# Kernel optimization log

Hardware: AMD Instinct MI355X
Metric: run time of the kernel (lower is better)

The kernel has to match this reference:

```python
import jax, jax.numpy as jnp
import numpy as np
from functools import partial

GRAD_THR = 0.01
COUNT_THR = 3
MIN_PROB = 0.1
MAX_PROB = 0.9
FREE_PROB = 1e-10
HEIGHT_Q = 0.7


def prob2logodds(p):
    return jnp.log(p) - jnp.log1p(-p)


def shift_diff(x, d):
    # right neighbor minus left neighbor at dilation d (replicate padding on width)
    xp = jnp.pad(x, [(0, 0)] * (x.ndim - 1) + [(d, d)], mode='edge')
    return xp[..., 2 * d:] - xp[..., :-2 * d]


def assign_score(depth):
    rml_dx = jax.nn.relu(shift_diff(depth, 1))    # relu(right - left)
    lmr_dx = jax.nn.relu(-shift_diff(depth, 1))   # relu(left - right)
    rml_ddx = jax.nn.relu(-shift_diff(rml_dx, 2))  # relu(-(right-left))
    lmr_ddx = jax.nn.relu(shift_diff(lmr_dx, 2))   # relu(-(left-right))
    W = depth.shape[-1]
    grad_pos = jnp.concatenate([rml_ddx[..., :W // 2], lmr_ddx[..., W // 2:]], axis=-1)
    grad_neg = jnp.concatenate([lmr_ddx[..., :W // 2], rml_ddx[..., W // 2:]], axis=-1)
    return grad_pos, grad_neg


def _occupancy_one(xyz, score, g_mask, size, grad_thr, count_thr):
    # xyz: [3, N]; score, g_mask: [N]
    x, y, z = xyz[0], xyz[1], xyz[2]
    range_mask = (x >= 0) & (x <= size - 1) & (z >= 0) & (z <= size - 1)
    height_mask = y < jnp.quantile(y, HEIGHT_Q)
    valid = height_mask & range_mask
    obj = valid & (~g_mask) & (score > 0)
    ground = valid & g_mask
    xi = jnp.clip(x.astype(jnp.int32), 0, size - 1)
    zi = jnp.clip(z.astype(jnp.int32), 0, size - 1)
    idx = xi + size * zi  # [N] flat grid index
    G = size * size
    occ = jnp.zeros(G, jnp.float32).at[idx].add(
        jnp.where(obj & (score > grad_thr), 1.0, 0.0))
    norm = jnp.zeros(G, jnp.float32).at[idx].add(obj.astype(jnp.float32))
    gcnt = jnp.zeros(G, jnp.float32).at[idx].add(ground.astype(jnp.float32))
    free = (gcnt > 0) & (norm == 0)
    unknown = (~free) & (norm < count_thr)
    prob = occ / jnp.maximum(norm, 1.0)
    prob = jnp.where(unknown | free, 0.5, prob)
    return prob, free, unknown


def compute_occupancy_probability(scaled_ptcloud, ground_flat, disc_flat, size, grad_thr, count_thr):
    f = partial(_occupancy_one, size=size, grad_thr=grad_thr, count_thr=count_thr)
    return jax.vmap(f)(scaled_ptcloud, disc_flat, ground_flat)


def max_pool3x3(x):
    return jax.lax.reduce_window(
        x, -jnp.inf, jax.lax.max,
        (1, 1, 3, 3), (1, 1, 1, 1),
        [(0, 0), (0, 0), (1, 1), (1, 1)])


def setup_inputs() -> dict:
    key = jax.random.key(0)
    k1, k2, k3 = jax.random.split(key, 3)
    B, H, W, S = 32, 384, 1280, 256
    N = H * W
    depth = jax.random.uniform(k1, (B, 1, H, W), jnp.float32, 0.1, 80.0)
    ptc = jax.random.uniform(k2, (B, 3, N), jnp.float32, -5.0, float(S) + 5.0)
    gmask = jax.random.randint(k3, (B, 1, H, W), 0, 2).astype(bool)
    return {"depth": depth, "scaled_ptcloud": ptc, "ground_mask": gmask, "ogm_size": S}


def reference(depth, scaled_ptcloud, ground_mask, ogm_size):
    B = depth.shape[0]
    S = ogm_size
    prior_free_odds = prob2logodds(FREE_PROB)
    p_min_odds = prob2logodds(MIN_PROB)
    p_max_odds = prob2logodds(MAX_PROB)
    n_max_odds = prob2logodds(MAX_PROB)

    grad_pos, grad_neg = assign_score(depth)
    gp_flat = grad_pos.reshape(B, -1)
    gn_flat = grad_neg.reshape(B, -1)
    gm_flat = ground_mask.reshape(B, -1)

    pos_prob, free, unknown = compute_occupancy_probability(
        scaled_ptcloud, gm_flat, gp_flat, S, GRAD_THR, COUNT_THR)
    pos_odds = prob2logodds(pos_prob)
    pos_odds = jnp.where(free, prior_free_odds, pos_odds)
    pos_odds = jnp.where(unknown, 0.0, pos_odds)
    pos_odds = jnp.clip(pos_odds, p_min_odds, p_max_odds)

    neg_prob, _, _ = compute_occupancy_probability(
        scaled_ptcloud, gm_flat, gn_flat, S, GRAD_THR, COUNT_THR)
    neg_odds = prob2logodds(neg_prob)
    neg_odds = jnp.where(free | unknown, 0.0, neg_odds)
    neg_odds = jnp.clip(neg_odds, 0.0, n_max_odds)
    neg_odds = max_pool3x3(neg_odds.reshape(B, 1, S, S))

    return pos_odds.reshape(B, 1, S, S) - neg_odds
```

## Files before the change

kernel.cpp:

```cpp
#include <hip/hip_runtime.h>
#include <stdint.h>

#define H_    384
#define W_    1280
#define NPTS  (H_ * W_)
#define S_    256
#define G_    (S_ * S_)
#define NBX   32
#define NBINS 4096
#define QCAP  4096
#define NT_Q  1024
#define LO_   (-16.0f)
#define INVW_ (4096.0f / 544.0f)
#define PMAX  2.1972246f

typedef unsigned int u32;
typedef unsigned long long u64;
typedef unsigned char u8;

__device__ __forceinline__ u32 fkey(float f) {
    u32 u = __float_as_uint(f);
    return (u & 0x80000000u) ? ~u : (u | 0x80000000u);
}
__device__ __forceinline__ float keyfloat(u32 k) {
    u32 u = (k & 0x80000000u) ? (k ^ 0x80000000u) : ~k;
    return __uint_as_float(u);
}
__device__ __forceinline__ int lbin(float y) {
    int b = (int)floorf((y - LO_) * INVW_);
    return b < 0 ? 0 : (b > NBINS - 1 ? NBINS - 1 : b);
}

__global__ void k_histlin(const float* __restrict__ ptc, const u8* __restrict__ gmb,
                          u32* __restrict__ hg, u32* __restrict__ mode) {
    __shared__ u32 h[NBINS];
    const int t = threadIdx.x, b = blockIdx.y;
    if (blockIdx.x == 0 && b == 0 && t < 64) {
        u32 v = ((const u32*)gmb)[t];
        bool bad = !(v == 0u || v == 1u || v == 0x3F800000u);
        u64 m = __ballot(bad);
        if (t == 0) *mode = (m == 0ULL) ? 1u : 0u;
    }
    for (int j = t; j < NBINS; j += 256) h[j] = 0u;
    __syncthreads();
    const float4* y4 = (const float4*)(ptc + (size_t)b * 3 * NPTS + NPTS);
    for (int i = blockIdx.x * 256 + t; i < NPTS / 4; i += NBX * 256) {
        float4 v = y4[i];
        atomicAdd(&h[lbin(v.x)], 1u);
        atomicAdd(&h[lbin(v.y)], 1u);
        atomicAdd(&h[lbin(v.z)], 1u);
        atomicAdd(&h[lbin(v.w)], 1u);
    }
    __syncthreads();
    u32* dst = hg + ((size_t)b * NBX + blockIdx.x) * NBINS;
    for (int j = t; j < NBINS; j += 256) dst[j] = h[j];
}

__global__ __launch_bounds__(NT_Q) void k_quant(const float* __restrict__ ptc,
                                                const u32* __restrict__ hg,
                                                float* __restrict__ tbuf,
                                                int ka, float wlo, float whi) {
    __shared__ u32 h[NBINS];
    __shared__ u32 part[NT_Q];
    __shared__ u32 bufA[QCAP];
    __shared__ u32 bufB[QCAP];
    __shared__ u32 sres[6];
    __shared__ u32 ca, cb;
    const int t = threadIdx.x, b = blockIdx.x;

    for (int j = t; j < NBINS; j += NT_Q) {
        u32 s = 0;
        for (int k = 0; k < NBX; k++) s += hg[((size_t)b * NBX + k) * NBINS + j];
        h[j] = s;
    }
    if (t == 0) { ca = 0u; cb = 0u; }
    __syncthreads();

    u32 loc = 0;
#pragma unroll
    for (int q = 0; q < NBINS / NT_Q; q++) loc += h[t * (NBINS / NT_Q) + q];
    part[t] = loc;
    __syncthreads();
    for (int ofs = 1; ofs < NT_Q; ofs <<= 1) {
        u32 v = (t >= ofs) ? part[t - ofs] : 0u;
        __syncthreads();
        part[t] += v;
        __syncthreads();
    }
    u32 before = part[t] - loc;
    const u32 ra = (u32)ka, rb = (u32)ka + 1u;
#pragma unroll
    for (int q = 0; q < NBINS / NT_Q; q++) {
        const int j = t * (NBINS / NT_Q) + q;
        const u32 v = h[j];
        if (before <= ra && ra < before + v) { sres[0] = (u32)j; sres[1] = ra - before; }
        if (before <= rb && rb < before + v) { sres[2] = (u32)j; sres[3] = rb - before; }
        before += v;
    }
    __syncthreads();
    const int binA = (int)sres[0], binB = (int)sres[2];
    const u32 remA = sres[1], remB = sres[3];
    const bool twob = (binB != binA);

    const float4* y4 = (const float4*)(ptc + (size_t)b * 3 * NPTS + NPTS);
    for (int i = t; i < NPTS / 4; i += NT_Q) {
        float4 v = y4[i];
        float f[4] = {v.x, v.y, v.z, v.w};
#pragma unroll
        for (int q = 0; q < 4; q++) {
            const int bn = lbin(f[q]);
            if (bn == binA) {
                u32 p = atomicAdd(&ca, 1u);
                if (p < QCAP) bufA[p] = fkey(f[q]);
            } else if (twob && bn == binB) {
                u32 p = atomicAdd(&cb, 1u);
                if (p < QCAP) bufB[p] = fkey(f[q]);
            }
        }
    }
    __syncthreads();

    const u32 mA = ca < QCAP ? ca : QCAP;
    for (u32 i = t; i < mA; i += NT_Q) {
        const u32 k = bufA[i];
        u32 less = 0, eq = 0;
        for (u32 j = 0; j < mA; j++) { u32 kj = bufA[j]; less += (kj < k); eq += (kj == k); }
        if (less <= remA && remA < less + eq) sres[4] = k;
    }
    const u32* src = twob ? bufB : bufA;
    const u32 mB = twob ? (cb < QCAP ? cb : QCAP) : mA;
    for (u32 i = t; i < mB; i += NT_Q) {
        const u32 k = src[i];
        u32 less = 0, eq = 0;
        for (u32 j = 0; j < mB; j++) { u32 kj = src[j]; less += (kj < k); eq += (kj == k); }
        if (less <= remB && remB < less + eq) sres[5] = k;
    }
    __syncthreads();
    if (t == 0) {
        float ylo = keyfloat(sres[4]);
        float yhi = keyfloat(sres[5]);
        tbuf[b] = __fadd_rn(__fmul_rn(ylo, wlo), __fmul_rn(yhi, whi));
    }
}

__global__ void k_scatter(const float* __restrict__ depth, const float* __restrict__ ptc,
                          const u8* __restrict__ gmb, const float* __restrict__ tbuf,
                          const u32* __restrict__ mode,
                          u64* __restrict__ pk, u8* __restrict__ gflag) {
    __shared__ float st;
    __shared__ u32 smode;
    if (threadIdx.x == 0) { st = tbuf[blockIdx.y]; smode = *mode; }
    __syncthreads();
    const int b = blockIdx.y;
    const int i = blockIdx.x * 256 + threadIdx.x;
    const size_t pb = (size_t)b * 3 * NPTS;
    const float y = ptc[pb + NPTS + i];
    if (!(y < st)) return;
    const float x = ptc[pb + i];
    const float z = ptc[pb + 2 * NPTS + i];
    if (!(x >= 0.0f && x <= 255.0f && z >= 0.0f && z <= 255.0f)) return;
    const int cell = (int)x + S_ * (int)z;

    u32 g;
    if (smode) g = ((const u32*)gmb)[(size_t)b * NPTS + i];
    else       g = (u32)gmb[(size_t)b * NPTS + i];

    if (g) { gflag[(size_t)b * G_ + cell] = 1; return; }

    const int col = i % W_;
    const int r0  = i - col;
    int j1 = col - 2; if (j1 < 0) j1 = 0;
    int j2 = col + 2; if (j2 > W_ - 1) j2 = W_ - 1;
    int am = j1 - 1;  if (am < 0) am = 0;
    int ap = j1 + 1;  if (ap > W_ - 1) ap = W_ - 1;
    int bm = j2 - 1;  if (bm < 0) bm = 0;
    int bp = j2 + 1;  if (bp > W_ - 1) bp = W_ - 1;
    const float* drow = depth + (size_t)b * NPTS + r0;
    float a = drow[ap] - drow[am];
    float c = drow[bp] - drow[bm];
    float rml1 = fmaxf(a, 0.0f),  lmr1 = fmaxf(-a, 0.0f);
    float rml2 = fmaxf(c, 0.0f),  lmr2 = fmaxf(-c, 0.0f);
    float rddx = fmaxf(rml1 - rml2, 0.0f);
    float lddx = fmaxf(lmr2 - lmr1, 0.0f);
    float sp, sn;
    if (col < W_ / 2) { sp = rddx; sn = lddx; } else { sp = lddx; sn = rddx; }
    u64 p = (sp > 0.0f) ? (1ULL | ((u64)(sp > 0.01f) << 12)) : 0ULL;
    u64 n = (sn > 0.0f) ? ((1ULL << 24) | ((u64)(sn > 0.01f) << 36)) : 0ULL;
    const u64 inc = p | n;
    if (inc) atomicAdd(&pk[(size_t)b * G_ + cell], inc);
}

#define TX 64
#define TZ 16

__device__ __forceinline__ float neg_val(u64 w) {
    const u32 pn = (u32)w & 0xFFFu;
    if (pn < 3u) return 0.0f;
    const u32 nn = (u32)(w >> 24) & 0xFFFu;
    if (nn < 3u) return 0.0f;
    const u32 no = (u32)(w >> 36) & 0xFFFu;
    float p = (float)no / (float)nn;
    float v = logf(p) - log1pf(-p);
    return fminf(fmaxf(v, 0.0f), PMAX);
}

__global__ void k_finalpool(const u64* __restrict__ pk, const u8* __restrict__ gflag,
                            float* __restrict__ out) {
    __shared__ float ng[(TZ + 2) * (TX + 2)];
    const int t = threadIdx.x, b = blockIdx.y;
    const int x0 = (blockIdx.x & 3) * TX;
    const int z0 = (blockIdx.x >> 2) * TZ;
    const u64* pkb = pk + (size_t)b * G_;
    const u8* gfb = gflag + (size_t)b * G_;
    for (int idx = t; idx < (TZ + 2) * (TX + 2); idx += 256) {
        const int gx = x0 + idx % (TX + 2) - 1;
        const int gz = z0 + idx / (TX + 2) - 1;
        float v = -INFINITY;
        if (gx >= 0 && gx < S_ && gz >= 0 && gz < S_) v = neg_val(pkb[gx + S_ * gz]);
        ng[idx] = v;
    }
    __syncthreads();
    const int lx = t & 63;
    const int lz0 = (t >> 6) * 4;
#pragma unroll
    for (int k = 0; k < 4; k++) {
        const int lz = lz0 + k;
        const int cell = (x0 + lx) + S_ * (z0 + lz);
        const u64 w = pkb[cell];
        const u32 pn = (u32)w & 0xFFFu;
        float po;
        if (pn < 3u) {
            po = (pn == 0u && gfb[cell]) ? -PMAX : 0.0f;
        } else {
            const u32 oc = (u32)(w >> 12) & 0xFFFu;
            float p = (float)oc / (float)pn;
            float v = logf(p) - log1pf(-p);
            po = fminf(fmaxf(v, -PMAX), PMAX);
        }
        float mx = -INFINITY;
#pragma unroll
        for (int dz = 0; dz < 3; dz++)
#pragma unroll
            for (int dx = 0; dx < 3; dx++)
                mx = fmaxf(mx, ng[(lz + dz) * (TX + 2) + (lx + dx)]);
        out[(size_t)b * G_ + cell] = po - mx;
    }
}

extern "C" void kernel_launch(void* const* d_in, const int* in_sizes, int n_in,
                              void* d_out, int out_size, void* d_ws, size_t ws_size,
                              hipStream_t stream) {
    const float* depth = (const float*)d_in[0];
    const float* ptc   = (const float*)d_in[1];
    const u8* gm       = (const u8*)d_in[2];
    const int B = in_sizes[0] / NPTS;

    char* ws = (char*)d_ws;
    size_t off = 0;
    auto alloc = [&](size_t bytes) -> void* {
        void* p = ws + off; off += (bytes + 255) & ~(size_t)255; return p;
    };
    u64* pk     = (u64*)alloc((size_t)B * G_ * 8);
    u8*  gflag  = (u8*)alloc((size_t)B * G_);
    const size_t zero_bytes = off;
    u32* hg     = (u32*)alloc((size_t)B * NBX * NBINS * 4);
    float* tbuf = (float*)alloc((size_t)B * 4);
    u32* mode   = (u32*)alloc(4);
    (void)ws_size;

    hipMemsetAsync(d_ws, 0, zero_bytes, stream);

    const float idxf = 0.7f * (float)(NPTS - 1);
    const int   ka   = (int)floorf(idxf);
    const float whi  = idxf - (float)ka;
    const float wlo  = 1.0f - whi;

    k_histlin <<<dim3(NBX, B), dim3(256), 0, stream>>>(ptc, gm, hg, mode);
    k_quant   <<<dim3(B), dim3(NT_Q), 0, stream>>>(ptc, hg, tbuf, ka, wlo, whi);
    k_scatter <<<dim3(NPTS / 256, B), dim3(256), 0, stream>>>(
        depth, ptc, gm, tbuf, mode, pk, gflag);
    k_finalpool<<<dim3(64, B), dim3(256), 0, stream>>>(pk, gflag, (float*)d_out);
}
```

Measured before the change: 535.2 us.

## Split quantile selection into parallel collect/select kernels and pack counters in u32

The single-block-per-batch quantile kernel is split into four stages. A global atomic histogram merge replaces the per-block partial histograms, a small prefix-search kernel finds the bins, a multi-block pass collects candidate keys into global buffers, and a select kernel ranks them from shared memory. This removes the serial full-point-cloud scan done by one block per batch. The scatter kernel now processes four points per thread with vector nontemporal loads. Cell counters are packed into 32-bit words with 8-bit fields instead of 64-bit words with 12-bit fields, which risks overflow if a cell receives 256 or more points. QCAP is also halved.

```diff
diff --git a/kernel.cpp b/kernel.cpp
--- a/kernel.cpp
+++ b/kernel.cpp
@@ -8,8 +8,7 @@
 #define G_    (S_ * S_)
 #define NBX   32
 #define NBINS 4096
-#define QCAP  4096
-#define NT_Q  1024
+#define QCAP  2048
 #define LO_   (-16.0f)
 #define INVW_ (4096.0f / 544.0f)
 #define PMAX  2.1972246f
@@ -17,6 +16,8 @@
 typedef unsigned int u32;
 typedef unsigned long long u64;
 typedef unsigned char u8;
+typedef float f32x4 __attribute__((ext_vector_type(4)));
+typedef u32   u32x4 __attribute__((ext_vector_type(4)));
 
 __device__ __forceinline__ u32 fkey(float f) {
     u32 u = __float_as_uint(f);
@@ -32,7 +33,7 @@
 }
 
 __global__ void k_histlin(const float* __restrict__ ptc, const u8* __restrict__ gmb,
-                          u32* __restrict__ hg, u32* __restrict__ mode) {
+                          u32* __restrict__ hgsum, u32* __restrict__ mode) {
     __shared__ u32 h[NBINS];
     const int t = threadIdx.x, b = blockIdx.y;
     if (blockIdx.x == 0 && b == 0 && t < 64) {
@@ -43,45 +44,34 @@
     }
     for (int j = t; j < NBINS; j += 256) h[j] = 0u;
     __syncthreads();
-    const float4* y4 = (const float4*)(ptc + (size_t)b * 3 * NPTS + NPTS);
+    const f32x4* y4 = (const f32x4*)(ptc + (size_t)b * 3 * NPTS + NPTS);
     for (int i = blockIdx.x * 256 + t; i < NPTS / 4; i += NBX * 256) {
-        float4 v = y4[i];
+        f32x4 v = y4[i];
         atomicAdd(&h[lbin(v.x)], 1u);
         atomicAdd(&h[lbin(v.y)], 1u);
         atomicAdd(&h[lbin(v.z)], 1u);
         atomicAdd(&h[lbin(v.w)], 1u);
     }
     __syncthreads();
-    u32* dst = hg + ((size_t)b * NBX + blockIdx.x) * NBINS;
-    for (int j = t; j < NBINS; j += 256) dst[j] = h[j];
-}
-
-__global__ __launch_bounds__(NT_Q) void k_quant(const float* __restrict__ ptc,
-                                                const u32* __restrict__ hg,
-                                                float* __restrict__ tbuf,
-                                                int ka, float wlo, float whi) {
+    u32* dst = hgsum + (size_t)b * NBINS;
+    for (int j = t; j < NBINS; j += 256)
+        if (h[j]) atomicAdd(&dst[j], h[j]);
+}
+
+__global__ void k_find(const u32* __restrict__ hgsum, u32* __restrict__ fbuf, int ka) {
     __shared__ u32 h[NBINS];
-    __shared__ u32 part[NT_Q];
-    __shared__ u32 bufA[QCAP];
-    __shared__ u32 bufB[QCAP];
-    __shared__ u32 sres[6];
-    __shared__ u32 ca, cb;
+    __shared__ u32 part[256];
+    __shared__ u32 sres[4];
     const int t = threadIdx.x, b = blockIdx.x;
-
-    for (int j = t; j < NBINS; j += NT_Q) {
-        u32 s = 0;
-        for (int k = 0; k < NBX; k++) s += hg[((size_t)b * NBX + k) * NBINS + j];
-        h[j] = s;
-    }
-    if (t == 0) { ca = 0u; cb = 0u; }
-    __syncthreads();
-
+    const u32* src = hgsum + (size_t)b * NBINS;
+    for (int j = t; j < NBINS; j += 256) h[j] = src[j];
+    __syncthreads();
     u32 loc = 0;
 #pragma unroll
-    for (int q = 0; q < NBINS / NT_Q; q++) loc += h[t * (NBINS / NT_Q) + q];
+    for (int q = 0; q < NBINS / 256; q++) loc += h[t * (NBINS / 256) + q];
     part[t] = loc;
     __syncthreads();
-    for (int ofs = 1; ofs < NT_Q; ofs <<= 1) {
+    for (int ofs = 1; ofs < 256; ofs <<= 1) {
         u32 v = (t >= ofs) ? part[t - ofs] : 0u;
         __syncthreads();
         part[t] += v;
@@ -90,127 +80,174 @@
     u32 before = part[t] - loc;
     const u32 ra = (u32)ka, rb = (u32)ka + 1u;
 #pragma unroll
-    for (int q = 0; q < NBINS / NT_Q; q++) {
-        const int j = t * (NBINS / NT_Q) + q;
+    for (int q = 0; q < NBINS / 256; q++) {
+        const int j = t * (NBINS / 256) + q;
         const u32 v = h[j];
         if (before <= ra && ra < before + v) { sres[0] = (u32)j; sres[1] = ra - before; }
         if (before <= rb && rb < before + v) { sres[2] = (u32)j; sres[3] = rb - before; }
         before += v;
     }
     __syncthreads();
-    const int binA = (int)sres[0], binB = (int)sres[2];
-    const u32 remA = sres[1], remB = sres[3];
+    if (t < 4) fbuf[b * 4 + t] = sres[t];
+}
+
+__global__ void k_collect(const float* __restrict__ ptc, const u32* __restrict__ fbuf,
+                          u32* __restrict__ cnt, u32* __restrict__ cbuf) {
+    __shared__ u32 sA, sB;
+    const int t = threadIdx.x, b = blockIdx.y;
+    if (t == 0) { sA = fbuf[b * 4 + 0]; sB = fbuf[b * 4 + 2]; }
+    __syncthreads();
+    const int binA = (int)sA, binB = (int)sB;
     const bool twob = (binB != binA);
-
-    const float4* y4 = (const float4*)(ptc + (size_t)b * 3 * NPTS + NPTS);
-    for (int i = t; i < NPTS / 4; i += NT_Q) {
-        float4 v = y4[i];
+    const f32x4* y4 = (const f32x4*)(ptc + (size_t)b * 3 * NPTS + NPTS);
+    u32* bufA = cbuf + (size_t)b * 2 * QCAP;
+    u32* bufB = bufA + QCAP;
+    for (int i = blockIdx.x * 256 + t; i < NPTS / 4; i += NBX * 256) {
+        f32x4 v = y4[i];
         float f[4] = {v.x, v.y, v.z, v.w};
 #pragma unroll
         for (int q = 0; q < 4; q++) {
             const int bn = lbin(f[q]);
             if (bn == binA) {
-                u32 p = atomicAdd(&ca, 1u);
+                u32 p = atomicAdd(&cnt[b * 2], 1u);
                 if (p < QCAP) bufA[p] = fkey(f[q]);
             } else if (twob && bn == binB) {
-                u32 p = atomicAdd(&cb, 1u);
+                u32 p = atomicAdd(&cnt[b * 2 + 1], 1u);
                 if (p < QCAP) bufB[p] = fkey(f[q]);
             }
         }
     }
-    __syncthreads();
-
-    const u32 mA = ca < QCAP ? ca : QCAP;
-    for (u32 i = t; i < mA; i += NT_Q) {
-        const u32 k = bufA[i];
+}
+
+__global__ void k_select(const u32* __restrict__ fbuf, const u32* __restrict__ cnt,
+                         const u32* __restrict__ cbuf, float* __restrict__ tbuf,
+                         float wlo, float whi) {
+    __shared__ u32 sA[QCAP];
+    __shared__ u32 sB[QCAP];
+    __shared__ u32 skey[2];
+    const int t = threadIdx.x, b = blockIdx.x;
+    const u32 binA = fbuf[b * 4 + 0], remA = fbuf[b * 4 + 1];
+    const u32 binB = fbuf[b * 4 + 2], remB = fbuf[b * 4 + 3];
+    const bool twob = (binB != binA);
+    u32 cA = cnt[b * 2];     if (cA > QCAP) cA = QCAP;
+    u32 cB = cnt[b * 2 + 1]; if (cB > QCAP) cB = QCAP;
+    const u32* bufA = cbuf + (size_t)b * 2 * QCAP;
+    const u32* bufB = bufA + QCAP;
+    for (u32 i = t; i < cA; i += 256) sA[i] = bufA[i];
+    if (twob) for (u32 i = t; i < cB; i += 256) sB[i] = bufB[i];
+    __syncthreads();
+    for (u32 i = t; i < cA; i += 256) {
+        const u32 k = sA[i];
         u32 less = 0, eq = 0;
-        for (u32 j = 0; j < mA; j++) { u32 kj = bufA[j]; less += (kj < k); eq += (kj == k); }
-        if (less <= remA && remA < less + eq) sres[4] = k;
-    }
-    const u32* src = twob ? bufB : bufA;
-    const u32 mB = twob ? (cb < QCAP ? cb : QCAP) : mA;
-    for (u32 i = t; i < mB; i += NT_Q) {
+        for (u32 j = 0; j < cA; j++) { u32 kj = sA[j]; less += (kj < k); eq += (kj == k); }
+        if (less <= remA && remA < less + eq) skey[0] = k;
+    }
+    const u32* src = twob ? sB : sA;
+    const u32 mB = twob ? cB : cA;
+    for (u32 i = t; i < mB; i += 256) {
         const u32 k = src[i];
         u32 less = 0, eq = 0;
         for (u32 j = 0; j < mB; j++) { u32 kj = src[j]; less += (kj < k); eq += (kj == k); }
-        if (less <= remB && remB < less + eq) sres[5] = k;
+        if (less <= remB && remB < less + eq) skey[1] = k;
     }
     __syncthreads();
     if (t == 0) {
-        float ylo = keyfloat(sres[4]);
-        float yhi = keyfloat(sres[5]);
+        float ylo = keyfloat(skey[0]);
+        float yhi = keyfloat(skey[1]);
         tbuf[b] = __fadd_rn(__fmul_rn(ylo, wlo), __fmul_rn(yhi, whi));
     }
+    (void)binA;
 }
 
 __global__ void k_scatter(const float* __restrict__ depth, const float* __restrict__ ptc,
                           const u8* __restrict__ gmb, const float* __restrict__ tbuf,
                           const u32* __restrict__ mode,
-                          u64* __restrict__ pk, u8* __restrict__ gflag) {
+                          u32* __restrict__ pk, u8* __restrict__ gflag) {
     __shared__ float st;
     __shared__ u32 smode;
     if (threadIdx.x == 0) { st = tbuf[blockIdx.y]; smode = *mode; }
     __syncthreads();
     const int b = blockIdx.y;
-    const int i = blockIdx.x * 256 + threadIdx.x;
+    const int i4 = blockIdx.x * 256 + threadIdx.x;
+    const int i0 = i4 * 4;
     const size_t pb = (size_t)b * 3 * NPTS;
-    const float y = ptc[pb + NPTS + i];
-    if (!(y < st)) return;
-    const float x = ptc[pb + i];
-    const float z = ptc[pb + 2 * NPTS + i];
-    if (!(x >= 0.0f && x <= 255.0f && z >= 0.0f && z <= 255.0f)) return;
-    const int cell = (int)x + S_ * (int)z;
-
-    u32 g;
-    if (smode) g = ((const u32*)gmb)[(size_t)b * NPTS + i];
-    else       g = (u32)gmb[(size_t)b * NPTS + i];
-
-    if (g) { gflag[(size_t)b * G_ + cell] = 1; return; }
-
-    const int col = i % W_;
-    const int r0  = i - col;
-    int j1 = col - 2; if (j1 < 0) j1 = 0;
-    int j2 = col + 2; if (j2 > W_ - 1) j2 = W_ - 1;
-    int am = j1 - 1;  if (am < 0) am = 0;
-    int ap = j1 + 1;  if (ap > W_ - 1) ap = W_ - 1;
-    int bm = j2 - 1;  if (bm < 0) bm = 0;
-    int bp = j2 + 1;  if (bp > W_ - 1) bp = W_ - 1;
-    const float* drow = depth + (size_t)b * NPTS + r0;
-    float a = drow[ap] - drow[am];
-    float c = drow[bp] - drow[bm];
-    float rml1 = fmaxf(a, 0.0f),  lmr1 = fmaxf(-a, 0.0f);
-    float rml2 = fmaxf(c, 0.0f),  lmr2 = fmaxf(-c, 0.0f);
-    float rddx = fmaxf(rml1 - rml2, 0.0f);
-    float lddx = fmaxf(lmr2 - lmr1, 0.0f);
-    float sp, sn;
-    if (col < W_ / 2) { sp = rddx; sn = lddx; } else { sp = lddx; sn = rddx; }
-    u64 p = (sp > 0.0f) ? (1ULL | ((u64)(sp > 0.01f) << 12)) : 0ULL;
-    u64 n = (sn > 0.0f) ? ((1ULL << 24) | ((u64)(sn > 0.01f) << 36)) : 0ULL;
-    const u64 inc = p | n;
-    if (inc) atomicAdd(&pk[(size_t)b * G_ + cell], inc);
+
+    const f32x4 yv = __builtin_nontemporal_load((const f32x4*)(ptc + pb + NPTS) + i4);
+    const float fy[4] = {yv.x, yv.y, yv.z, yv.w};
+    bool pass[4]; bool any = false;
+#pragma unroll
+    for (int q = 0; q < 4; q++) { pass[q] = fy[q] < st; any = any || pass[q]; }
+    if (!any) return;
+
+    const f32x4 xv = __builtin_nontemporal_load((const f32x4*)(ptc + pb) + i4);
+    const f32x4 zv = __builtin_nontemporal_load((const f32x4*)(ptc + pb + 2 * NPTS) + i4);
+    const float fx[4] = {xv.x, xv.y, xv.z, xv.w};
+    const float fz[4] = {zv.x, zv.y, zv.z, zv.w};
+    u32 gw[4];
+    if (smode) {
+        u32x4 gg = __builtin_nontemporal_load((const u32x4*)((const u32*)gmb + (size_t)b * NPTS) + i4);
+        gw[0] = gg.x; gw[1] = gg.y; gw[2] = gg.z; gw[3] = gg.w;
+    } else {
+        u32 gg = __builtin_nontemporal_load((const u32*)(gmb + (size_t)b * NPTS) + i4);
+        gw[0] = gg & 0xFFu; gw[1] = (gg >> 8) & 0xFFu; gw[2] = (gg >> 16) & 0xFFu; gw[3] = (gg >> 24) & 0xFFu;
+    }
+
+    const int colbase = i0 % W_;
+    const float* drow = depth + (size_t)b * NPTS + (i0 - colbase);
+    u32* pkb = pk + (size_t)b * G_;
+    u8* gfb = gflag + (size_t)b * G_;
+
+#pragma unroll
+    for (int q = 0; q < 4; q++) {
+        if (!pass[q]) continue;
+        const float x = fx[q], z = fz[q];
+        if (!(x >= 0.0f && x <= 255.0f && z >= 0.0f && z <= 255.0f)) continue;
+        const int cell = (int)x + S_ * (int)z;
+        if (gw[q]) { gfb[cell] = 1; continue; }
+
+        const int col = colbase + q;
+        int j1 = col - 2; if (j1 < 0) j1 = 0;
+        int j2 = col + 2; if (j2 > W_ - 1) j2 = W_ - 1;
+        int am = j1 - 1;  if (am < 0) am = 0;
+        int ap = j1 + 1;  if (ap > W_ - 1) ap = W_ - 1;
+        int bm = j2 - 1;  if (bm < 0) bm = 0;
+        int bp = j2 + 1;  if (bp > W_ - 1) bp = W_ - 1;
+        float a = drow[ap] - drow[am];
+        float c = drow[bp] - drow[bm];
+        float rml1 = fmaxf(a, 0.0f),  lmr1 = fmaxf(-a, 0.0f);
+        float rml2 = fmaxf(c, 0.0f),  lmr2 = fmaxf(-c, 0.0f);
+        float rddx = fmaxf(rml1 - rml2, 0.0f);
+        float lddx = fmaxf(lmr2 - lmr1, 0.0f);
+        float sp, sn;
+        if (col < W_ / 2) { sp = rddx; sn = lddx; } else { sp = lddx; sn = rddx; }
+        u32 p = (sp > 0.0f) ? (1u | ((u32)(sp > 0.01f) << 8)) : 0u;
+        u32 n = (sn > 0.0f) ? ((1u << 16) | ((u32)(sn > 0.01f) << 24)) : 0u;
+        const u32 inc = p | n;
+        if (inc) atomicAdd(&pkb[cell], inc);
+    }
 }
 
 #define TX 64
 #define TZ 16
 
-__device__ __forceinline__ float neg_val(u64 w) {
-    const u32 pn = (u32)w & 0xFFFu;
+__device__ __forceinline__ float neg_val(u32 w) {
+    const u32 pn = w & 0xFFu;
     if (pn < 3u) return 0.0f;
-    const u32 nn = (u32)(w >> 24) & 0xFFFu;
+    const u32 nn = (w >> 16) & 0xFFu;
     if (nn < 3u) return 0.0f;
-    const u32 no = (u32)(w >> 36) & 0xFFFu;
+    const u32 no = (w >> 24) & 0xFFu;
     float p = (float)no / (float)nn;
     float v = logf(p) - log1pf(-p);
     return fminf(fmaxf(v, 0.0f), PMAX);
 }
 
-__global__ void k_finalpool(const u64* __restrict__ pk, const u8* __restrict__ gflag,
+__global__ void k_finalpool(const u32* __restrict__ pk, const u8* __restrict__ gflag,
                             float* __restrict__ out) {
     __shared__ float ng[(TZ + 2) * (TX + 2)];
     const int t = threadIdx.x, b = blockIdx.y;
     const int x0 = (blockIdx.x & 3) * TX;
     const int z0 = (blockIdx.x >> 2) * TZ;
-    const u64* pkb = pk + (size_t)b * G_;
+    const u32* pkb = pk + (size_t)b * G_;
     const u8* gfb = gflag + (size_t)b * G_;
     for (int idx = t; idx < (TZ + 2) * (TX + 2); idx += 256) {
         const int gx = x0 + idx % (TX + 2) - 1;
@@ -226,13 +263,13 @@
     for (int k = 0; k < 4; k++) {
         const int lz = lz0 + k;
         const int cell = (x0 + lx) + S_ * (z0 + lz);
-        const u64 w = pkb[cell];
-        const u32 pn = (u32)w & 0xFFFu;
+        const u32 w = pkb[cell];
+        const u32 pn = w & 0xFFu;
         float po;
         if (pn < 3u) {
             po = (pn == 0u && gfb[cell]) ? -PMAX : 0.0f;
         } else {
-            const u32 oc = (u32)(w >> 12) & 0xFFFu;
+            const u32 oc = (w >> 8) & 0xFFu;
             float p = (float)oc / (float)pn;
             float v = logf(p) - log1pf(-p);
             po = fminf(fmaxf(v, -PMAX), PMAX);
@@ -260,24 +297,29 @@
     auto alloc = [&](size_t bytes) -> void* {
         void* p = ws + off; off += (bytes + 255) & ~(size_t)255; return p;
     };
-    u64* pk     = (u64*)alloc((size_t)B * G_ * 8);
-    u8*  gflag  = (u8*)alloc((size_t)B * G_);
+    u32* pk    = (u32*)alloc((size_t)B * G_ * 4);
+    u8*  gflag = (u8*)alloc((size_t)B * G_);
+    u32* hgsum = (u32*)alloc((size_t)B * NBINS * 4);
+    u32* cnt   = (u32*)alloc((size_t)B * 2 * 4);
     const size_t zero_bytes = off;
-    u32* hg     = (u32*)alloc((size_t)B * NBX * NBINS * 4);
-    float* tbuf = (float*)alloc((size_t)B * 4);
-    u32* mode   = (u32*)alloc(4);
-    (void)ws_size;
-
-    hipMemsetAsync(d_ws, 0, zero_bytes, stream);
+    u32* cbuf  = (u32*)alloc((size_t)B * 2 * QCAP * 4);
+    float* tbuf= (float*)alloc((size_t)B * 4);
+    u32* fbuf  = (u32*)alloc((size_t)B * 4 * 4);
+    u32* mode  = (u32*)alloc(4);
+    (void)ws_size; (void)n_in; (void)out_size;
+
+    (void)hipMemsetAsync(d_ws, 0, zero_bytes, stream);
 
     const float idxf = 0.7f * (float)(NPTS - 1);
     const int   ka   = (int)floorf(idxf);
     const float whi  = idxf - (float)ka;
     const float wlo  = 1.0f - whi;
 
-    k_histlin <<<dim3(NBX, B), dim3(256), 0, stream>>>(ptc, gm, hg, mode);
-    k_quant   <<<dim3(B), dim3(NT_Q), 0, stream>>>(ptc, hg, tbuf, ka, wlo, whi);
-    k_scatter <<<dim3(NPTS / 256, B), dim3(256), 0, stream>>>(
+    k_histlin <<<dim3(NBX, B), dim3(256), 0, stream>>>(ptc, gm, hgsum, mode);
+    k_find    <<<dim3(B), dim3(256), 0, stream>>>(hgsum, fbuf, ka);
+    k_collect <<<dim3(NBX, B), dim3(256), 0, stream>>>(ptc, fbuf, cnt, cbuf);
+    k_select  <<<dim3(B), dim3(256), 0, stream>>>(fbuf, cnt, cbuf, tbuf, wlo, whi);
+    k_scatter <<<dim3(NPTS / 1024, B), dim3(256), 0, stream>>>(
         depth, ptc, gm, tbuf, mode, pk, gflag);
     k_finalpool<<<dim3(64, B), dim3(256), 0, stream>>>(pk, gflag, (float*)d_out);
 }
```

After: 507.9 us. 5.1% less time.
